# Performance work log

Measured on AMD Instinct MI355X. Metric: run time of the kernel, lower is better.

Reference implementation:

```python
import jax, jax.numpy as jnp
import numpy as np

N, S, IN_F, TEXT_D, EMB, H = 128, 1024, 768, 512, 512, 8
HD = EMB // H  # 64


def setup_inputs() -> dict:
    key = jax.random.key(0)
    ks = jax.random.split(key, 14)
    sc = 0.02
    return {
        "v": jax.random.normal(ks[0], (1, N, 12, IN_F), dtype=jnp.float32),
        "t": jax.random.normal(ks[1], (N, S, TEXT_D), dtype=jnp.float32),
        "t_len": jax.random.randint(ks[2], (N,), 1, S + 1, dtype=jnp.int32),
        "W_fc1": jax.random.normal(ks[3], (EMB, IN_F), dtype=jnp.float32) * sc,
        "b_fc1": jnp.zeros((EMB,), jnp.float32),
        "W_fc2": jax.random.normal(ks[4], (EMB, 12 * EMB), dtype=jnp.float32) * sc,
        "b_fc2": jnp.zeros((EMB,), jnp.float32),
        "Wq": jax.random.normal(ks[5], (EMB, EMB), dtype=jnp.float32) * sc,
        "Wk": jax.random.normal(ks[6], (EMB, TEXT_D), dtype=jnp.float32) * sc,
        "Wv": jax.random.normal(ks[7], (EMB, TEXT_D), dtype=jnp.float32) * sc,
        "bq": jnp.zeros((EMB,), jnp.float32),
        "bk": jnp.zeros((EMB,), jnp.float32),
        "bv": jnp.zeros((EMB,), jnp.float32),
        "Wo": jax.random.normal(ks[8], (EMB, EMB), dtype=jnp.float32) * sc,
        "bo": jnp.zeros((EMB,), jnp.float32),
    }


def reference(v, t, t_len, W_fc1, b_fc1, W_fc2, b_fc2, Wq, Wk, Wv, bq, bk, bv, Wo, bo):
    # fc1 + ReLU: [1,N,12,IN_F] -> [N,12,EMB]
    x = jax.nn.relu(jnp.einsum('onif,ef->onie', v, W_fc1) + b_fc1)[0]
    # flatten + fc2 + ReLU -> [N, EMB]
    x = x.reshape(N, 12 * EMB)
    vfeat = jax.nn.relu(x @ W_fc2.T + b_fc2)
    # Batched ragged multihead attention, query length 1 per item.
    scale = 1.0 / jnp.sqrt(jnp.asarray(HD, vfeat.dtype))
    q = ((vfeat @ Wq.T + bq) * scale).reshape(N, H, HD)           # [N,H,HD]
    k = (jnp.einsum('nsd,ed->nse', t, Wk) + bk).reshape(N, S, H, HD)
    vv = (jnp.einsum('nsd,ed->nse', t, Wv) + bv).reshape(N, S, H, HD)
    scores = jnp.einsum('nhd,nshd->nhs', q, k)                    # [N,H,S]
    valid = (jnp.arange(S)[None, :] < t_len[:, None])[:, None, :]  # [N,1,S]
    scores = jnp.where(valid, scores, jnp.finfo(scores.dtype).min)
    w = jax.nn.softmax(scores, axis=-1)                           # [N,H,S]
    ctx = jnp.einsum('nhs,nshd->nhd', w, vv).reshape(N, EMB)
    attn_out = ctx @ Wo.T + bo                                    # [N,EMB]
    return vfeat, attn_out
```

## Files before the change

kernel.cpp:

```cpp
#include <hip/hip_runtime.h>

#define NB 128
#define SSEQ 1024
#define TD 512

typedef _Float16 half8 __attribute__((ext_vector_type(8)));
typedef _Float16 half4 __attribute__((ext_vector_type(4)));
typedef float f32x4 __attribute__((ext_vector_type(4)));

template<int AM, int BM>
__global__ __launch_bounds__(256) void k_gemm(
    const void* __restrict__ Av, int lda, long aSZ,
    const void* __restrict__ Bv, int ldb, long bSZ,
    const float* __restrict__ bias, const float* __restrict__ aRowScale,
    float scale, int doRelu, int outMode,
    float* __restrict__ outF, _Float16* __restrict__ outH,
    int ldc, int cColOff, int mtiles, int kTiles, long oSplit)
{
  __shared__ _Float16 As[64][72];
  __shared__ _Float16 Bs[64][72];
  int mt = blockIdx.x % mtiles, nt = blockIdx.x / mtiles;
  int sp = blockIdx.y, bz = blockIdx.z;
  int tid = threadIdx.x;
  int r = tid >> 2, kq = (tid & 3) * 16;
  int w = tid >> 6, l = tid & 63;
  long aoff = (long)bz * aSZ + (long)(mt * 64 + r) * lda + (long)sp * kTiles * 64 + kq;
  long boff = (long)bz * bSZ + (long)(nt * 64 + r) * ldb + (long)sp * kTiles * 64 + kq;
  const _Float16* apH = (const _Float16*)Av + aoff;
  const float*    apF = (const float*)Av + aoff;
  const _Float16* bpH = (const _Float16*)Bv + boff;
  const float*    bpF = (const float*)Bv + boff;
  float srA = 1.0f;
  if constexpr (AM == 2) srA = 1.0f / aRowScale[(mt * 64 + r) * 8 + bz];

  half8 pa0, pa1, pb0, pb1;
  f32x4 qa0, qa1, qa2, qa3, qc0, qc1, qc2, qc3;
  if constexpr (AM == 0) { pa0 = *(const half8*)apH; pa1 = *(const half8*)(apH + 8); }
  else { qa0 = *(const f32x4*)apF; qa1 = *(const f32x4*)(apF + 4);
         qa2 = *(const f32x4*)(apF + 8); qa3 = *(const f32x4*)(apF + 12); }
  if constexpr (BM == 0) { pb0 = *(const half8*)bpH; pb1 = *(const half8*)(bpH + 8); }
  else { qc0 = *(const f32x4*)bpF; qc1 = *(const f32x4*)(bpF + 4);
         qc2 = *(const f32x4*)(bpF + 8); qc3 = *(const f32x4*)(bpF + 12); }

  f32x4 acc[4];
  #pragma unroll
  for (int c = 0; c < 4; ++c) acc[c] = (f32x4){0.f, 0.f, 0.f, 0.f};
  int fr = l & 15, fo = (l >> 4) * 8;
  for (int kt = 0; kt < kTiles; ++kt) {
    __syncthreads();
    if constexpr (AM == 0) {
      *(half8*)&As[r][kq] = pa0; *(half8*)&As[r][kq + 8] = pa1;
    } else {
      f32x4 s0 = qa0, s1 = qa1, s2 = qa2, s3 = qa3;
      if constexpr (AM == 2) { s0 *= srA; s1 *= srA; s2 *= srA; s3 *= srA; }
      *(half4*)&As[r][kq + 0]  = __builtin_convertvector(s0, half4);
      *(half4*)&As[r][kq + 4]  = __builtin_convertvector(s1, half4);
      *(half4*)&As[r][kq + 8]  = __builtin_convertvector(s2, half4);
      *(half4*)&As[r][kq + 12] = __builtin_convertvector(s3, half4);
    }
    if constexpr (BM == 0) {
      *(half8*)&Bs[r][kq] = pb0; *(half8*)&Bs[r][kq + 8] = pb1;
    } else {
      *(half4*)&Bs[r][kq + 0]  = __builtin_convertvector(qc0, half4);
      *(half4*)&Bs[r][kq + 4]  = __builtin_convertvector(qc1, half4);
      *(half4*)&Bs[r][kq + 8]  = __builtin_convertvector(qc2, half4);
      *(half4*)&Bs[r][kq + 12] = __builtin_convertvector(qc3, half4);
    }
    __syncthreads();
    if (kt + 1 < kTiles) {
      apH += 64; apF += 64; bpH += 64; bpF += 64;
      if constexpr (AM == 0) { pa0 = *(const half8*)apH; pa1 = *(const half8*)(apH + 8); }
      else { qa0 = *(const f32x4*)apF; qa1 = *(const f32x4*)(apF + 4);
             qa2 = *(const f32x4*)(apF + 8); qa3 = *(const f32x4*)(apF + 12); }
      if constexpr (BM == 0) { pb0 = *(const half8*)bpH; pb1 = *(const half8*)(bpH + 8); }
      else { qc0 = *(const f32x4*)bpF; qc1 = *(const f32x4*)(bpF + 4);
             qc2 = *(const f32x4*)(bpF + 8); qc3 = *(const f32x4*)(bpF + 12); }
    }
    #pragma unroll
    for (int ks = 0; ks < 2; ++ks) {
      half8 af = *(const half8*)&As[16 * w + fr][ks * 32 + fo];
      #pragma unroll
      for (int c = 0; c < 4; ++c) {
        half8 bf = *(const half8*)&Bs[16 * c + fr][ks * 32 + fo];
        acc[c] = __builtin_amdgcn_mfma_f32_16x16x32_f16(af, bf, acc[c], 0, 0, 0);
      }
    }
  }
  int lrow = (l >> 4) * 4, lcol = l & 15;
  #pragma unroll
  for (int c = 0; c < 4; ++c) {
    #pragma unroll
    for (int rr = 0; rr < 4; ++rr) {
      int gm = mt * 64 + 16 * w + lrow + rr;
      int gn = nt * 64 + 16 * c + lcol;
      int ecol = gn + bz * cColOff;
      float vv = acc[c][rr];
      if (bias) vv += bias[ecol];
      vv *= scale;
      if (doRelu) vv = fmaxf(vv, 0.f);
      long oidx = (long)gm * ldc + ecol;
      if (outMode == 0) outF[oidx] = vv;
      else if (outMode == 1) outH[oidx] = (_Float16)vv;
      else outF[oidx + (long)sp * oSplit] = vv;
    }
  }
}

__global__ __launch_bounds__(256) void k_vfeat(
    const float* __restrict__ vacc, const float* __restrict__ b2,
    float* __restrict__ outF, _Float16* __restrict__ vf16)
{
  int i = blockIdx.x * 256 + threadIdx.x;
  float vv = b2[i & 511];
  #pragma unroll
  for (int sp = 0; sp < 16; ++sp) vv += vacc[sp * 65536 + i];
  vv = fmaxf(vv, 0.f);
  outF[i] = vv;
  vf16[i] = (_Float16)vv;
}

__global__ __launch_bounds__(256) void k_qk(
    const float* __restrict__ qf, const float* __restrict__ Wk,
    const float* __restrict__ bk, _Float16* __restrict__ qk16, float* __restrict__ qb)
{
  int n = blockIdx.x, tid = threadIdx.x;
  __shared__ float qs[512];
  qs[tid] = qf[n * 512 + tid];
  qs[tid + 256] = qf[n * 512 + tid + 256];
  __syncthreads();
  _Float16* qn = qk16 + (long)n * 8192;
  #pragma unroll 1
  for (int h = 0; h < 8; ++h) {
    float a0 = 0.f, a1 = 0.f;
    #pragma unroll 8
    for (int j = 0; j < 64; ++j) {
      float qv = qs[h * 64 + j];
      const float* wr = Wk + (long)(h * 64 + j) * 512;
      a0 = fmaf(qv, wr[tid], a0);
      a1 = fmaf(qv, wr[tid + 256], a1);
    }
    qn[h * 512 + tid] = (_Float16)a0;
    qn[h * 512 + tid + 256] = (_Float16)a1;
  }
  #pragma unroll
  for (int h = 8; h < 16; ++h) {
    qn[h * 512 + tid] = (_Float16)0.f;
    qn[h * 512 + tid + 256] = (_Float16)0.f;
  }
  if (tid < 64) {
    #pragma unroll 1
    for (int h = 0; h < 8; ++h) {
      float pb = qs[h * 64 + tid] * bk[h * 64 + tid];
      #pragma unroll
      for (int m = 1; m < 64; m <<= 1) pb += __shfl_xor(pb, m, 64);
      if (tid == 0) qb[n * 8 + h] = pb;
    }
  }
}

__global__ __launch_bounds__(256) void k_attn(
    const float* __restrict__ t, const int* __restrict__ tlen,
    const _Float16* __restrict__ qk16, const float* __restrict__ qb,
    float* __restrict__ pu, float* __restrict__ pl)
{
  int n = blockIdx.x >> 4, j = blockIdx.x & 15;
  int len = tlen[n];
  int base0 = j * 64;
  if (base0 >= len) return;
  int tid = threadIdx.x, wid = tid >> 6, l = tid & 63;
  int fr = l & 15, fo = (l >> 4) * 8;

  __shared__ __align__(16) _Float16 ts[32][520];
  __shared__ __align__(16) _Float16 wst[16][32];
  __shared__ float lred[8];
  if (tid < 8) lred[tid] = 0.f;

  const float* tn = t + (long)n * SSEQ * TD;
  const _Float16* qn = qk16 + (long)n * 8192 + fr * 512 + fo;
  float qbr = (fr < 8) ? qb[n * 8 + fr] : 0.f;

  f32x4 upv[8];
  #pragma unroll
  for (int dt = 0; dt < 8; ++dt) upv[dt] = (f32x4){0.f, 0.f, 0.f, 0.f};

  #pragma unroll 1
  for (int sub = 0; sub < 2; ++sub) {
    int base = base0 + sub * 32;
    if (base >= len) break;
    int s1 = base + 32; if (s1 > len) s1 = len;
    __syncthreads();
    {
      f32x4 a0, a1, b0, b1;
      auto ld = [&](int c, f32x4& x0, f32x4& x1) {
        int sg = base + c * 4 + wid;
        if (sg < s1) {
          const float* p = tn + (long)sg * TD;
          x0 = *(const f32x4*)(p + 4 * l);
          x1 = *(const f32x4*)(p + 256 + 4 * l);
        } else {
          x0 = (f32x4){0.f,0.f,0.f,0.f}; x1 = (f32x4){0.f,0.f,0.f,0.f};
        }
      };
      ld(0, a0, a1); ld(1, b0, b1);
      #pragma unroll
      for (int c = 0; c < 8; c += 2) {
        half4 h0 = __builtin_convertvector(a0, half4);
        half4 h1 = __builtin_convertvector(a1, half4);
        int row = c * 4 + wid;
        if (c + 2 < 8) ld(c + 2, a0, a1);
        *(half4*)&ts[row][4 * l] = h0;
        *(half4*)&ts[row][256 + 4 * l] = h1;
        half4 g0 = __builtin_convertvector(b0, half4);
        half4 g1 = __builtin_convertvector(b1, half4);
        int row2 = c * 4 + 4 + wid;
        if (c + 3 < 8) ld(c + 3, b0, b1);
        *(half4*)&ts[row2][4 * l] = g0;
        *(half4*)&ts[row2][256 + 4 * l] = g1;
      }
    }
    __syncthreads();
    if (wid < 2) {
      f32x4 acc = (f32x4){0.f, 0.f, 0.f, 0.f};
      #pragma unroll 4
      for (int kt = 0; kt < 16; ++kt) {
        half8 bf = *(const half8*)(qn + kt * 32);
        half8 af = *(const half8*)&ts[16 * wid + fr][kt * 32 + fo];
        acc = __builtin_amdgcn_mfma_f32_16x16x32_f16(af, bf, acc, 0, 0, 0);
      }
      float lac = 0.f;
      #pragma unroll
      for (int r = 0; r < 4; ++r) {
        int sl = 16 * wid + (l >> 4) * 4 + r;
        float wv = (fr < 8 && base + sl < s1) ? __expf(acc[r] + qbr) : 0.f;
        wst[fr][sl] = (_Float16)wv;
        lac += wv;
      }
      if (fr < 8) atomicAdd(&lred[fr], lac);
    }
    __syncthreads();
    {
      half8 af = *(const half8*)&wst[fr][fo];
      #pragma unroll
      for (int dt = 0; dt < 8; ++dt) {
        int dcol = 128 * wid + dt * 16 + fr;
        half8 bf;
        #pragma unroll
        for (int jj = 0; jj < 8; ++jj) bf[jj] = ts[fo + jj][dcol];
        upv[dt] = __builtin_amdgcn_mfma_f32_16x16x32_f16(af, bf, upv[dt], 0, 0, 0);
      }
    }
  }
  int quad = l >> 4;
  float* pn = pu + (long)n * 4096;
  if (quad < 2) {
    #pragma unroll
    for (int dt = 0; dt < 8; ++dt) {
      int d = 128 * wid + dt * 16 + fr;
      #pragma unroll
      for (int r = 0; r < 4; ++r)
        atomicAdd(&pn[(quad * 4 + r) * 512 + d], upv[dt][r]);
    }
  }
  if (tid < 8) atomicAdd(&pl[n * 8 + tid], lred[tid]);
}

extern "C" void kernel_launch(void* const* d_in, const int* in_sizes, int n_in,
                              void* d_out, int out_size, void* d_ws, size_t ws_size,
                              hipStream_t stream)
{
  const float* v    = (const float*)d_in[0];
  const float* t    = (const float*)d_in[1];
  const int*   tlen = (const int*)d_in[2];
  const float* W1   = (const float*)d_in[3];
  const float* b1   = (const float*)d_in[4];
  const float* W2   = (const float*)d_in[5];
  const float* b2   = (const float*)d_in[6];
  const float* Wq   = (const float*)d_in[7];
  const float* Wk   = (const float*)d_in[8];
  const float* Wv   = (const float*)d_in[9];
  const float* bq   = (const float*)d_in[10];
  const float* bk   = (const float*)d_in[11];
  const float* bv   = (const float*)d_in[12];
  const float* Wo   = (const float*)d_in[13];
  const float* bo   = (const float*)d_in[14];
  float* out = (float*)d_out;

  _Float16* hb   = (_Float16*)d_ws;
  _Float16* x16  = hb;
  _Float16* vf16 = hb + 786432l;
  _Float16* ctx16= hb + 851968l;
  _Float16* qk16 = hb + 917504l;
  float* fb   = (float*)(hb + 1966080l);
  float* vacc = fb;
  float* qf   = fb + 1048576l;
  float* pu   = fb + 1114112l;
  float* pl   = fb + 1638400l;
  float* qb   = fb + 1639424l;

  hipMemsetAsync(pu, 0, (524288l + 1024l) * sizeof(float), stream);
  k_gemm<1,1><<<dim3(192, 1, 1), 256, 0, stream>>>(v, 768, 0, W1, 768, 0,
      b1, nullptr, 1.f, 1, 1, nullptr, x16, 512, 0, 24, 12, 0);
  k_gemm<0,1><<<dim3(16, 16, 1), 256, 0, stream>>>(x16, 6144, 0, W2, 6144, 0,
      nullptr, nullptr, 1.f, 0, 2, vacc, nullptr, 512, 0, 2, 6, 65536);
  k_vfeat<<<256, 256, 0, stream>>>(vacc, b2, out, vf16);
  k_gemm<0,1><<<dim3(16, 1, 1), 256, 0, stream>>>(vf16, 512, 0, Wq, 512, 0,
      bq, nullptr, 0.125f, 0, 0, qf, nullptr, 512, 0, 2, 8, 0);
  k_qk<<<128, 256, 0, stream>>>(qf, Wk, bk, qk16, qb);
  k_attn<<<NB * 16, 256, 0, stream>>>(t, tlen, qk16, qb, pu, pl);
  k_gemm<2,1><<<dim3(2, 1, 8), 256, 0, stream>>>(pu, 4096, 512, Wv, 512, 32768,
      bv, pl, 1.f, 0, 1, nullptr, ctx16, 512, 64, 2, 8, 0);
  k_gemm<0,1><<<dim3(16, 1, 1), 256, 0, stream>>>(ctx16, 512, 0, Wo, 512, 0,
      bo, nullptr, 1.f, 0, 0, out + 65536, nullptr, 512, 0, 2, 8, 0);
}
```

Baseline: 491.3 us.

## Precompose Wq·Wk per head so query-key projection is one GEMM

Adds a prep kernel that builds the per-head product of Wq and Wk (scaled, stored in fp16), plus the bias-derived vectors. The per-sample projected query is then one batched GEMM from vfeat instead of a q GEMM followed by a scalar per-sample loop over Wk. The prep kernel also zeroes the partial buffers and the padded query region, replacing the memset. This removes the slow per-sample k_qk kernel, but the prep work depends only on weights and is redone on every call, and computing from fp16 vfeat through an fp16 composed matrix may change rounding.

```diff
diff --git a/kernel.cpp b/kernel.cpp
--- a/kernel.cpp
+++ b/kernel.cpp
@@ -106,6 +106,80 @@
   }
 }
 
+__global__ __launch_bounds__(256) void k_prep(
+    const float* __restrict__ Wq, const float* __restrict__ Wk,
+    const float* __restrict__ bq, const float* __restrict__ bk,
+    _Float16* __restrict__ G16T, float* __restrict__ gb,
+    float* __restrict__ qbc, float* __restrict__ cvec,
+    float* __restrict__ pz, _Float16* __restrict__ qz)
+{
+  int b = blockIdx.x, tid = threadIdx.x;
+  int gid = b * 256 + tid;
+  for (long i = gid; i < 131328; i += 131072)
+    *(f32x4*)(pz + 4 * i) = (f32x4){0.f, 0.f, 0.f, 0.f};
+  {
+    long i4 = (long)gid * 4;
+    long n = i4 >> 12, off = i4 & 4095;
+    *(half4*)(qz + n * 8192 + 4096 + off) = (half4){(_Float16)0, (_Float16)0, (_Float16)0, (_Float16)0};
+  }
+  int h = b >> 6, et = (b >> 3) & 7, dt = b & 7;
+  __shared__ float Aq[64][68];
+  __shared__ float Bk[64][68];
+  __shared__ float bqs[64], bks[64];
+  int r = tid >> 2, cq = (tid & 3) * 16;
+  const float* wqp = Wq + (long)(h * 64 + r) * 512 + et * 64 + cq;
+  const float* wkp = Wk + (long)(h * 64 + r) * 512 + dt * 64 + cq;
+  #pragma unroll
+  for (int c = 0; c < 4; ++c) {
+    *(f32x4*)&Aq[r][cq + 4 * c] = *(const f32x4*)(wqp + 4 * c);
+    *(f32x4*)&Bk[r][cq + 4 * c] = *(const f32x4*)(wkp + 4 * c);
+  }
+  if (tid < 64) { bqs[tid] = bq[h * 64 + tid]; bks[tid] = bk[h * 64 + tid]; }
+  __syncthreads();
+  int te = tid & 15, td = tid >> 4;
+  float acc[4][4];
+  #pragma unroll
+  for (int a = 0; a < 4; ++a)
+    #pragma unroll
+    for (int d = 0; d < 4; ++d) acc[a][d] = 0.f;
+  #pragma unroll 4
+  for (int j = 0; j < 64; ++j) {
+    f32x4 av = *(const f32x4*)&Aq[j][te * 4];
+    f32x4 bv = *(const f32x4*)&Bk[j][td * 4];
+    #pragma unroll
+    for (int a = 0; a < 4; ++a)
+      #pragma unroll
+      for (int d = 0; d < 4; ++d) acc[a][d] = fmaf(av[a], bv[d], acc[a][d]);
+  }
+  #pragma unroll
+  for (int d = 0; d < 4; ++d) {
+    half4 hv = { (_Float16)(0.125f * acc[0][d]), (_Float16)(0.125f * acc[1][d]),
+                 (_Float16)(0.125f * acc[2][d]), (_Float16)(0.125f * acc[3][d]) };
+    *(half4*)(G16T + (long)h * 262144 + (long)(dt * 64 + td * 4 + d) * 512 + et * 64 + te * 4) = hv;
+  }
+  if (dt == 0 && td == 0) {
+    #pragma unroll
+    for (int i = 0; i < 4; ++i) {
+      float s = 0.f;
+      for (int j = 0; j < 64; ++j) s = fmaf(Aq[j][te * 4 + i], bks[j], s);
+      gb[h * 512 + et * 64 + te * 4 + i] = 0.125f * s;
+    }
+  }
+  if (et == 0 && te == 0) {
+    #pragma unroll
+    for (int i = 0; i < 4; ++i) {
+      float s = 0.f;
+      for (int j = 0; j < 64; ++j) s = fmaf(Bk[j][td * 4 + i], bqs[j], s);
+      cvec[h * 512 + dt * 64 + td * 4 + i] = 0.125f * s;
+    }
+  }
+  if (et == 0 && dt == 0 && tid == 0) {
+    float s = 0.f;
+    for (int j = 0; j < 64; ++j) s = fmaf(bqs[j], bks[j], s);
+    qbc[h] = 0.125f * s;
+  }
+}
+
 __global__ __launch_bounds__(256) void k_vfeat(
     const float* __restrict__ vacc, const float* __restrict__ b2,
     float* __restrict__ outF, _Float16* __restrict__ vf16)
@@ -119,43 +193,21 @@
   vf16[i] = (_Float16)vv;
 }
 
-__global__ __launch_bounds__(256) void k_qk(
-    const float* __restrict__ qf, const float* __restrict__ Wk,
-    const float* __restrict__ bk, _Float16* __restrict__ qk16, float* __restrict__ qb)
+__global__ __launch_bounds__(256) void k_qb(
+    const _Float16* __restrict__ vf16, const float* __restrict__ gb,
+    const float* __restrict__ qbc, float* __restrict__ qb)
 {
   int n = blockIdx.x, tid = threadIdx.x;
   __shared__ float qs[512];
-  qs[tid] = qf[n * 512 + tid];
-  qs[tid + 256] = qf[n * 512 + tid + 256];
+  qs[tid] = (float)vf16[n * 512 + tid];
+  qs[tid + 256] = (float)vf16[n * 512 + tid + 256];
   __syncthreads();
-  _Float16* qn = qk16 + (long)n * 8192;
-  #pragma unroll 1
-  for (int h = 0; h < 8; ++h) {
-    float a0 = 0.f, a1 = 0.f;
-    #pragma unroll 8
-    for (int j = 0; j < 64; ++j) {
-      float qv = qs[h * 64 + j];
-      const float* wr = Wk + (long)(h * 64 + j) * 512;
-      a0 = fmaf(qv, wr[tid], a0);
-      a1 = fmaf(qv, wr[tid + 256], a1);
-    }
-    qn[h * 512 + tid] = (_Float16)a0;
-    qn[h * 512 + tid + 256] = (_Float16)a1;
-  }
-  #pragma unroll
-  for (int h = 8; h < 16; ++h) {
-    qn[h * 512 + tid] = (_Float16)0.f;
-    qn[h * 512 + tid + 256] = (_Float16)0.f;
-  }
-  if (tid < 64) {
-    #pragma unroll 1
-    for (int h = 0; h < 8; ++h) {
-      float pb = qs[h * 64 + tid] * bk[h * 64 + tid];
-      #pragma unroll
-      for (int m = 1; m < 64; m <<= 1) pb += __shfl_xor(pb, m, 64);
-      if (tid == 0) qb[n * 8 + h] = pb;
-    }
-  }
+  int h = tid >> 5, j = tid & 31;
+  float p = 0.f;
+  for (int e = j; e < 512; e += 32) p = fmaf(qs[e], gb[h * 512 + e], p);
+  #pragma unroll
+  for (int m = 1; m < 32; m <<= 1) p += __shfl_xor(p, m, 32);
+  if (j == 0) qb[n * 8 + h] = p + qbc[h];
 }
 
 __global__ __launch_bounds__(256) void k_attn(
@@ -290,22 +342,25 @@
   _Float16* vf16 = hb + 786432l;
   _Float16* ctx16= hb + 851968l;
   _Float16* qk16 = hb + 917504l;
-  float* fb   = (float*)(hb + 1966080l);
+  _Float16* G16T = hb + 1966080l;
+  float* fb   = (float*)(hb + 4063232l);
   float* vacc = fb;
-  float* qf   = fb + 1048576l;
-  float* pu   = fb + 1114112l;
-  float* pl   = fb + 1638400l;
-  float* qb   = fb + 1639424l;
-
-  hipMemsetAsync(pu, 0, (524288l + 1024l) * sizeof(float), stream);
+  float* pu   = fb + 1048576l;
+  float* pl   = fb + 1572864l;
+  float* qb   = fb + 1573888l;
+  float* gb   = fb + 1574912l;
+  float* qbc  = fb + 1579008l;
+  float* cvec = fb + 1579024l;
+
+  k_prep<<<512, 256, 0, stream>>>(Wq, Wk, bq, bk, G16T, gb, qbc, cvec, pu, qk16);
   k_gemm<1,1><<<dim3(192, 1, 1), 256, 0, stream>>>(v, 768, 0, W1, 768, 0,
       b1, nullptr, 1.f, 1, 1, nullptr, x16, 512, 0, 24, 12, 0);
   k_gemm<0,1><<<dim3(16, 16, 1), 256, 0, stream>>>(x16, 6144, 0, W2, 6144, 0,
       nullptr, nullptr, 1.f, 0, 2, vacc, nullptr, 512, 0, 2, 6, 65536);
   k_vfeat<<<256, 256, 0, stream>>>(vacc, b2, out, vf16);
-  k_gemm<0,1><<<dim3(16, 1, 1), 256, 0, stream>>>(vf16, 512, 0, Wq, 512, 0,
-      bq, nullptr, 0.125f, 0, 0, qf, nullptr, 512, 0, 2, 8, 0);
-  k_qk<<<128, 256, 0, stream>>>(qf, Wk, bk, qk16, qb);
+  k_gemm<0,0><<<dim3(16, 1, 8), 256, 0, stream>>>(vf16, 512, 0, G16T, 512, 262144,
+      cvec, nullptr, 1.f, 0, 1, nullptr, qk16, 8192, 512, 2, 8, 0);
+  k_qb<<<128, 256, 0, stream>>>(vf16, gb, qbc, qb);
   k_attn<<<NB * 16, 256, 0, stream>>>(t, tlen, qk16, qb, pu, pl);
   k_gemm<2,1><<<dim3(2, 1, 8), 256, 0, stream>>>(pu, 4096, 512, Wv, 512, 32768,
       bv, pl, 1.f, 0, 1, nullptr, ctx16, 512, 64, 2, 8, 0);
```

Measured after the change: 464.7 us. -5.4%, faster.
